# Optimization experiments

Measured on AMD Instinct MI355X. Metric: run time of the kernel, lower is better.

The kernel has to match this reference:

```python
import jax, jax.numpy as jnp
import numpy as np
import math

B, L, D = 4, 2048, 1024        # batch, x_len, x_dim
QKV, H = 64, 16                # qkv_dim, head_dim (number of heads)


def setup_inputs() -> dict:
    key = jax.random.key(0)
    ks = jax.random.split(key, 10)
    s = 1.0 / math.sqrt(D)
    return {
        "x": jax.random.normal(ks[0], (B, L, D), jnp.float32),
        "encoder_x": jax.random.normal(ks[1], (B, L, D), jnp.float32),
        "Wq": jax.random.normal(ks[2], (D, QKV * H), jnp.float32) * s,
        "bq": jax.random.normal(ks[3], (QKV * H,), jnp.float32) * 0.01,
        "Wk": jax.random.normal(ks[4], (D, QKV * H), jnp.float32) * s,
        "bk": jax.random.normal(ks[5], (QKV * H,), jnp.float32) * 0.01,
        "Wv": jax.random.normal(ks[6], (D, QKV * H), jnp.float32) * s,
        "bv": jax.random.normal(ks[7], (QKV * H,), jnp.float32) * 0.01,
        "Wo": jax.random.normal(ks[8], (QKV * H, D), jnp.float32) * s,
        "bo": jax.random.normal(ks[9], (D,), jnp.float32) * 0.01,
    }


def reference(x, encoder_x, Wq, bq, Wk, bk, Wv, bv, Wo, bo):
    # q,k from encoder_x; v from x  -> [B, L, H, QKV]
    q = (encoder_x @ Wq + bq).reshape(B, L, H, QKV)
    k = (encoder_x @ Wk + bk).reshape(B, L, H, QKV)
    v = (x @ Wv + bv).reshape(B, L, H, QKV)
    # explicit [B,H,L,L] score matrix + softmax over k (faithful to source)
    scores = jax.nn.softmax(
        jnp.einsum("bqhd,bkhd->bhqk", q, k) / math.sqrt(QKV), axis=-1
    )
    # faithful to source einsum 'bvhd,bhqk->bvhd': no shared contraction
    # index, so scores are summed over (q,k) and broadcast onto v per (b,h).
    attn = jnp.einsum("bvhd,bhqk->bvhd", v, scores).reshape(B, L, H * QKV)
    return attn @ Wo + bo
```

## Files before the change

kernel.cpp:

```cpp
#include <hip/hip_runtime.h>
#include <stdint.h>


typedef __attribute__((ext_vector_type(8))) short bf16x8;
typedef __attribute__((ext_vector_type(4))) float f32x4;

typedef __attribute__((address_space(1))) void as1_void;
typedef __attribute__((address_space(3))) void as3_void;
#define GLD16(g, s)                                                          \
  __builtin_amdgcn_global_load_lds((as1_void*)(g), (as3_void*)(s), 16, 0, 0)

__device__ __forceinline__ short f2bf(float f) {
  union { float f; uint32_t u; } v; v.f = f;
  uint32_t r = v.u + 0x7FFFu + ((v.u >> 16) & 1u);
  return (short)(r >> 16);
}

__device__ __forceinline__ bf16x8 pack8(f32x4 a, f32x4 b) {
  union { f32x4 f; uint32_t u[4]; } x, y;
  x.f = a; y.f = b;
#pragma unroll
  for (int t = 0; t < 4; ++t) x.u[t] += 0x8000u;
#pragma unroll
  for (int t = 0; t < 4; ++t) y.u[t] += 0x8000u;
  union { bf16x8 v; uint32_t u[4]; } o;
  o.u[0] = __builtin_amdgcn_perm(x.u[1], x.u[0], 0x07060302);
  o.u[1] = __builtin_amdgcn_perm(x.u[3], x.u[2], 0x07060302);
  o.u[2] = __builtin_amdgcn_perm(y.u[1], y.u[0], 0x07060302);
  o.u[3] = __builtin_amdgcn_perm(y.u[3], y.u[2], 0x07060302);
  return o.v;
}

__global__ __launch_bounds__(256) void prep(
    const float* __restrict__ x, short* __restrict__ x_bf,
    const float* __restrict__ Wo, short* __restrict__ wot,
    const float* __restrict__ bv, const float* __restrict__ bo,
    float* __restrict__ biasc) {
  constexpr int N = 1024, D = 1024;
  __shared__ union {
    float tile[64][65];
    float red[256];
  } sm;
  const int b = blockIdx.x, tid = threadIdx.x;

  if (b < 4096) {
    const int i = b * 256 + tid;
    const float4* p = (const float4*)x;
    float4 a = p[2 * (size_t)i], c = p[2 * (size_t)i + 1];
    bf16x8 o;
    o[0] = f2bf(a.x); o[1] = f2bf(a.y); o[2] = f2bf(a.z); o[3] = f2bf(a.w);
    o[4] = f2bf(c.x); o[5] = f2bf(c.y); o[6] = f2bf(c.z); o[7] = f2bf(c.w);
    *(bf16x8*)(x_bf + 8 * (size_t)i) = o;
  } else if (b < 4352) {
    const int b2 = b - 4096;
    const int br = (b2 >> 4) * 64, bc = (b2 & 15) * 64;
#pragma unroll
    for (int t = 0; t < 16; ++t) {
      int idx = t * 256 + tid;
      int r = idx >> 6, c = idx & 63;
      sm.tile[r][c] = Wo[(size_t)(br + r) * N + bc + c];
    }
    __syncthreads();
#pragma unroll
    for (int t = 0; t < 16; ++t) {
      int idx = t * 256 + tid;
      int r = idx >> 6, c = idx & 63;
      wot[(size_t)(bc + r) * N + br + c] = f2bf(sm.tile[c][r]);
    }
  } else {
    const int b3 = b - 4352;
    const int nx = tid & 15, ky = tid >> 4;
    const int n = b3 * 16 + nx;
    float s = 0.f;
    for (int k = ky; k < D; k += 16)
      s += bv[k] * Wo[(size_t)k * N + n];
    sm.red[tid] = s;
    __syncthreads();
#pragma unroll
    for (int st = 128; st >= 16; st >>= 1) {
      if (tid < st) sm.red[tid] += sm.red[tid + st];
      __syncthreads();
    }
    if (ky == 0) biasc[n] = 2048.0f * sm.red[nx] + bo[n];
  }
}

__global__ __launch_bounds__(256) void gemm_w(
    const short* __restrict__ Wot, const float* __restrict__ Wv,
    short* __restrict__ Wt, int N, int K) {
  constexpr int BK = 64;
  __shared__ __align__(16) short As[32 * BK];
  __shared__ __align__(16) float Bsf[64 * BK];
  const int tid = threadIdx.x, lane = tid & 63, wave = tid >> 6;
  const int bm = blockIdx.y * 32, bn = blockIdx.x * 64;
  const int wm = (wave & 1) * 16, wn = (wave >> 1) * 32;
  const int l15 = lane & 15, quad = lane >> 4;

  f32x4 acc[2];
  acc[0] = (f32x4){0.f, 0.f, 0.f, 0.f};
  acc[1] = (f32x4){0.f, 0.f, 0.f, 0.f};

  const int ar = tid >> 3, ac8 = (tid & 7) ^ (ar & 7);
  const short* pa = Wot + (size_t)(bm + ar) * K + ac8 * 8;
  short* la = As + tid * 8;
  const int br = tid >> 4, bc4 = (tid & 15) ^ (br & 7);
  const float* pb = Wv + (size_t)(bn + br) * K + bc4 * 4;
  float* lb = Bsf + tid * 4;

  for (int kt = 0; kt < K; kt += BK) {
    GLD16(pa, la);
#pragma unroll
    for (int s = 0; s < 4; ++s) GLD16(pb + (size_t)(16 * s) * K, lb + 1024 * s);
    pa += BK; pb += BK;
    __syncthreads();
#pragma unroll
    for (int kk = 0; kk < 2; ++kk) {
      const int r = wm + l15;
      bf16x8 af =
          *(const bf16x8*)(As + r * BK + ((kk * 4 + quad) ^ (r & 7)) * 8);
#pragma unroll
      for (int j = 0; j < 2; ++j) {
        const int rn = wn + j * 16 + l15;
        const int c4 = kk * 8 + quad * 2;
        f32x4 u0 = *(const f32x4*)(Bsf + (rn * 16 + (c4 ^ (rn & 7))) * 4);
        f32x4 u1 = *(const f32x4*)(Bsf + (rn * 16 + ((c4 + 1) ^ (rn & 7))) * 4);
        acc[j] = __builtin_amdgcn_mfma_f32_16x16x32_bf16(af, pack8(u0, u1),
                                                         acc[j], 0, 0, 0);
      }
    }
    __syncthreads();
  }
#pragma unroll
  for (int j = 0; j < 2; ++j) {
    const int col = bn + wn + j * 16 + l15;
    const int row0 = bm + wm + quad * 4;
#pragma unroll
    for (int r = 0; r < 4; ++r)
      Wt[(size_t)(row0 + r) * N + col] = f2bf(2048.f * acc[j][r]);
  }
}

__global__ __launch_bounds__(256) void gemm_main(
    const short* __restrict__ A, const short* __restrict__ Bt,
    const float* __restrict__ bias, float* __restrict__ Out,
    int M, int N, int K) {
  constexpr int BK = 64;
  __shared__ __align__(16) char smem[24576];
  short* As = (short*)smem;
  short* Bs = (short*)(smem + 16384);
  const int tid = threadIdx.x, lane = tid & 63, wave = tid >> 6;
  const int b = blockIdx.x;
  const int bm = (b & 63) * 128;
  const int bn = (b >> 6) * 64;
  const int wm = (wave & 1) * 64, wn = (wave >> 1) * 32;
  const int l15 = lane & 15, quad = lane >> 4;

  f32x4 acc[4][2];
#pragma unroll
  for (int i = 0; i < 4; ++i)
#pragma unroll
    for (int j = 0; j < 2; ++j) acc[i][j] = (f32x4){0.f, 0.f, 0.f, 0.f};

  const int srow = tid >> 3, sc8 = (tid & 7) ^ (srow & 7);
  const short* pa = A + (size_t)(bm + srow) * K + sc8 * 8;
  const short* pb = Bt + (size_t)(bn + srow) * K + sc8 * 8;
  short* la = As + tid * 8;
  short* lb = Bs + tid * 8;

  for (int kt = 0; kt < K; kt += BK) {
#pragma unroll
    for (int s = 0; s < 4; ++s) GLD16(pa + (size_t)(32 * s) * K, la + 2048 * s);
#pragma unroll
    for (int s = 0; s < 2; ++s) GLD16(pb + (size_t)(32 * s) * K, lb + 2048 * s);
    pa += BK; pb += BK;
    __syncthreads();
#pragma unroll
    for (int kk = 0; kk < 2; ++kk) {
      bf16x8 af[4], bfr[2];
#pragma unroll
      for (int i = 0; i < 4; ++i) {
        const int r = wm + i * 16 + l15;
        af[i] = *(const bf16x8*)(As + r * BK + ((kk * 4 + quad) ^ (r & 7)) * 8);
      }
#pragma unroll
      for (int j = 0; j < 2; ++j) {
        const int r = wn + j * 16 + l15;
        bfr[j] = *(const bf16x8*)(Bs + r * BK + ((kk * 4 + quad) ^ (r & 7)) * 8);
      }
#pragma unroll
      for (int i = 0; i < 4; ++i)
#pragma unroll
        for (int j = 0; j < 2; ++j)
          acc[i][j] = __builtin_amdgcn_mfma_f32_16x16x32_bf16(
              af[i], bfr[j], acc[i][j], 0, 0, 0);
    }
    __syncthreads();
  }

  float* T = (float*)smem + wave * 576;
#pragma unroll
  for (int i = 0; i < 4; ++i) {
#pragma unroll
    for (int j = 0; j < 2; ++j) {
      const float bb = bias[bn + wn + j * 16 + l15];
#pragma unroll
      for (int r = 0; r < 4; ++r)
        T[(quad * 4 + r) * 36 + j * 16 + l15] = acc[i][j][r] + bb;
    }
#pragma unroll
    for (int c = 0; c < 2; ++c) {
      const int row = (lane >> 3) + 8 * c;
      f32x4 v = *(const f32x4*)(T + row * 36 + (lane & 7) * 4);
      *(f32x4*)(Out + (size_t)(bm + wm + i * 16 + row) * N + bn + wn +
                (lane & 7) * 4) = v;
    }
  }
}

extern "C" void kernel_launch(void* const* d_in, const int* in_sizes, int n_in,
                              void* d_out, int out_size, void* d_ws,
                              size_t ws_size, hipStream_t stream) {
  const float* x  = (const float*)d_in[0];
  const float* Wv = (const float*)d_in[6];
  const float* bv = (const float*)d_in[7];
  const float* Wo = (const float*)d_in[8];
  const float* bo = (const float*)d_in[9];
  float* out = (float*)d_out;

  constexpr int L = 2048, D = 1024, NO = 1024;
  constexpr int M = 4 * L;

  char* ws = (char*)d_ws;
  short* x_bf   = (short*)(ws);
  short* wot_bf = (short*)(ws + (16u << 20));
  short* wt_bf  = (short*)(ws + (18u << 20));
  float* biasc  = (float*)(ws + (20u << 20));

  prep<<<4416, 256, 0, stream>>>(x, x_bf, Wo, wot_bf, bv, bo, biasc);
  gemm_w<<<dim3(16, 32), 256, 0, stream>>>(wot_bf, Wv, wt_bf, NO, D);
  gemm_main<<<(M / 128) * (NO / 64), 256, 0, stream>>>(
      x_bf, wt_bf, biasc, out, M, NO, D);
}
```

Measured before the change: 181.0 us.

## Widen main GEMM tile to 128x128 and overlap x conversion with weight GEMM

```diff
diff --git a/kernel.cpp b/kernel.cpp
--- a/kernel.cpp
+++ b/kernel.cpp
@@ -31,8 +31,7 @@
   return o.v;
 }
 
-__global__ __launch_bounds__(256) void prep(
-    const float* __restrict__ x, short* __restrict__ x_bf,
+__global__ __launch_bounds__(256) void prep_w(
     const float* __restrict__ Wo, short* __restrict__ wot,
     const float* __restrict__ bv, const float* __restrict__ bo,
     float* __restrict__ biasc) {
@@ -43,56 +42,61 @@
   } sm;
   const int b = blockIdx.x, tid = threadIdx.x;
 
-  if (b < 4096) {
-    const int i = b * 256 + tid;
+  if (b < 256) {
+    const int br = (b >> 4) * 64, bc = (b & 15) * 64;
+#pragma unroll
+    for (int t = 0; t < 16; ++t) {
+      int idx = t * 256 + tid;
+      int r = idx >> 6, c = idx & 63;
+      sm.tile[r][c] = Wo[(size_t)(br + r) * N + bc + c];
+    }
+    __syncthreads();
+#pragma unroll
+    for (int t = 0; t < 16; ++t) {
+      int idx = t * 256 + tid;
+      int r = idx >> 6, c = idx & 63;
+      wot[(size_t)(bc + r) * N + br + c] = f2bf(sm.tile[c][r]);
+    }
+  } else {
+    const int b3 = b - 256;
+    const int nx = tid & 15, ky = tid >> 4;
+    const int n = b3 * 16 + nx;
+    float s = 0.f;
+    for (int k = ky; k < D; k += 16)
+      s += bv[k] * Wo[(size_t)k * N + n];
+    sm.red[tid] = s;
+    __syncthreads();
+#pragma unroll
+    for (int st = 128; st >= 16; st >>= 1) {
+      if (tid < st) sm.red[tid] += sm.red[tid + st];
+      __syncthreads();
+    }
+    if (ky == 0) biasc[n] = 2048.0f * sm.red[nx] + bo[n];
+  }
+}
+
+__global__ __launch_bounds__(256) void mid(
+    const float* __restrict__ x, short* __restrict__ x_bf,
+    const short* __restrict__ Wot, const float* __restrict__ Wv,
+    short* __restrict__ Wt) {
+  constexpr int BK = 64, N = 1024, K = 1024;
+  __shared__ __align__(16) short As[32 * BK];
+  __shared__ __align__(16) float Bsf[64 * BK];
+  const int b = blockIdx.x, tid = threadIdx.x;
+
+  if (b >= 512) {
+    const int i = (b - 512) * 256 + tid;
     const float4* p = (const float4*)x;
     float4 a = p[2 * (size_t)i], c = p[2 * (size_t)i + 1];
     bf16x8 o;
     o[0] = f2bf(a.x); o[1] = f2bf(a.y); o[2] = f2bf(a.z); o[3] = f2bf(a.w);
     o[4] = f2bf(c.x); o[5] = f2bf(c.y); o[6] = f2bf(c.z); o[7] = f2bf(c.w);
     *(bf16x8*)(x_bf + 8 * (size_t)i) = o;
-  } else if (b < 4352) {
-    const int b2 = b - 4096;
-    const int br = (b2 >> 4) * 64, bc = (b2 & 15) * 64;
-#pragma unroll
-    for (int t = 0; t < 16; ++t) {
-      int idx = t * 256 + tid;
-      int r = idx >> 6, c = idx & 63;
-      sm.tile[r][c] = Wo[(size_t)(br + r) * N + bc + c];
-    }
-    __syncthreads();
-#pragma unroll
-    for (int t = 0; t < 16; ++t) {
-      int idx = t * 256 + tid;
-      int r = idx >> 6, c = idx & 63;
-      wot[(size_t)(bc + r) * N + br + c] = f2bf(sm.tile[c][r]);
-    }
-  } else {
-    const int b3 = b - 4352;
-    const int nx = tid & 15, ky = tid >> 4;
-    const int n = b3 * 16 + nx;
-    float s = 0.f;
-    for (int k = ky; k < D; k += 16)
-      s += bv[k] * Wo[(size_t)k * N + n];
-    sm.red[tid] = s;
-    __syncthreads();
-#pragma unroll
-    for (int st = 128; st >= 16; st >>= 1) {
-      if (tid < st) sm.red[tid] += sm.red[tid + st];
-      __syncthreads();
-    }
-    if (ky == 0) biasc[n] = 2048.0f * sm.red[nx] + bo[n];
-  }
-}
-
-__global__ __launch_bounds__(256) void gemm_w(
-    const short* __restrict__ Wot, const float* __restrict__ Wv,
-    short* __restrict__ Wt, int N, int K) {
-  constexpr int BK = 64;
-  __shared__ __align__(16) short As[32 * BK];
-  __shared__ __align__(16) float Bsf[64 * BK];
-  const int tid = threadIdx.x, lane = tid & 63, wave = tid >> 6;
-  const int bm = blockIdx.y * 32, bn = blockIdx.x * 64;
+    return;
+  }
+
+  const int lane = tid & 63, wave = tid >> 6;
+  const int bm = (b >> 4) * 32, bn = (b & 15) * 64;
   const int wm = (wave & 1) * 16, wn = (wave >> 1) * 32;
   const int l15 = lane & 15, quad = lane >> 4;
 
@@ -145,21 +149,21 @@
     const float* __restrict__ bias, float* __restrict__ Out,
     int M, int N, int K) {
   constexpr int BK = 64;
-  __shared__ __align__(16) char smem[24576];
+  __shared__ __align__(16) char smem[32768];
   short* As = (short*)smem;
   short* Bs = (short*)(smem + 16384);
   const int tid = threadIdx.x, lane = tid & 63, wave = tid >> 6;
   const int b = blockIdx.x;
   const int bm = (b & 63) * 128;
-  const int bn = (b >> 6) * 64;
-  const int wm = (wave & 1) * 64, wn = (wave >> 1) * 32;
+  const int bn = (b >> 6) * 128;
+  const int wm = (wave & 1) * 64, wn = (wave >> 1) * 64;
   const int l15 = lane & 15, quad = lane >> 4;
 
-  f32x4 acc[4][2];
+  f32x4 acc[4][4];
 #pragma unroll
   for (int i = 0; i < 4; ++i)
 #pragma unroll
-    for (int j = 0; j < 2; ++j) acc[i][j] = (f32x4){0.f, 0.f, 0.f, 0.f};
+    for (int j = 0; j < 4; ++j) acc[i][j] = (f32x4){0.f, 0.f, 0.f, 0.f};
 
   const int srow = tid >> 3, sc8 = (tid & 7) ^ (srow & 7);
   const short* pa = A + (size_t)(bm + srow) * K + sc8 * 8;
@@ -171,48 +175,49 @@
 #pragma unroll
     for (int s = 0; s < 4; ++s) GLD16(pa + (size_t)(32 * s) * K, la + 2048 * s);
 #pragma unroll
-    for (int s = 0; s < 2; ++s) GLD16(pb + (size_t)(32 * s) * K, lb + 2048 * s);
+    for (int s = 0; s < 4; ++s) GLD16(pb + (size_t)(32 * s) * K, lb + 2048 * s);
     pa += BK; pb += BK;
     __syncthreads();
 #pragma unroll
     for (int kk = 0; kk < 2; ++kk) {
-      bf16x8 af[4], bfr[2];
+      bf16x8 af[4], bfr[4];
 #pragma unroll
       for (int i = 0; i < 4; ++i) {
         const int r = wm + i * 16 + l15;
         af[i] = *(const bf16x8*)(As + r * BK + ((kk * 4 + quad) ^ (r & 7)) * 8);
       }
 #pragma unroll
-      for (int j = 0; j < 2; ++j) {
+      for (int j = 0; j < 4; ++j) {
         const int r = wn + j * 16 + l15;
         bfr[j] = *(const bf16x8*)(Bs + r * BK + ((kk * 4 + quad) ^ (r & 7)) * 8);
       }
 #pragma unroll
       for (int i = 0; i < 4; ++i)
 #pragma unroll
-        for (int j = 0; j < 2; ++j)
+        for (int j = 0; j < 4; ++j)
           acc[i][j] = __builtin_amdgcn_mfma_f32_16x16x32_bf16(
               af[i], bfr[j], acc[i][j], 0, 0, 0);
     }
     __syncthreads();
   }
 
-  float* T = (float*)smem + wave * 576;
+  float* T = (float*)smem + wave * 1088;
 #pragma unroll
   for (int i = 0; i < 4; ++i) {
 #pragma unroll
-    for (int j = 0; j < 2; ++j) {
+    for (int j = 0; j < 4; ++j) {
       const float bb = bias[bn + wn + j * 16 + l15];
 #pragma unroll
       for (int r = 0; r < 4; ++r)
-        T[(quad * 4 + r) * 36 + j * 16 + l15] = acc[i][j][r] + bb;
-    }
-#pragma unroll
-    for (int c = 0; c < 2; ++c) {
-      const int row = (lane >> 3) + 8 * c;
-      f32x4 v = *(const f32x4*)(T + row * 36 + (lane & 7) * 4);
+        T[(quad * 4 + r) * 68 + j * 16 + l15] = acc[i][j][r] + bb;
+    }
+#pragma unroll
+    for (int p = 0; p < 4; ++p) {
+      const int row = (lane >> 4) + 4 * p;
+      const int ch = lane & 15;
+      f32x4 v = *(const f32x4*)(T + row * 68 + ch * 4);
       *(f32x4*)(Out + (size_t)(bm + wm + i * 16 + row) * N + bn + wn +
-                (lane & 7) * 4) = v;
+                ch * 4) = v;
     }
   }
 }
@@ -236,8 +241,8 @@
   short* wt_bf  = (short*)(ws + (18u << 20));
   float* biasc  = (float*)(ws + (20u << 20));
 
-  prep<<<4416, 256, 0, stream>>>(x, x_bf, Wo, wot_bf, bv, bo, biasc);
-  gemm_w<<<dim3(16, 32), 256, 0, stream>>>(wot_bf, Wv, wt_bf, NO, D);
-  gemm_main<<<(M / 128) * (NO / 64), 256, 0, stream>>>(
+  prep_w<<<320, 256, 0, stream>>>(Wo, wot_bf, bv, bo, biasc);
+  mid<<<4608, 256, 0, stream>>>(x, x_bf, wot_bf, Wv, wt_bf);
+  gemm_main<<<(M / 128) * (NO / 128), 256, 0, stream>>>(
       x_bf, wt_bf, biasc, out, M, NO, D);
 }
```

Result: faster. 177.3 us (-2.0%).
